# Performance work log

Hardware: AMD Instinct MI355X
Metric: run time of the kernel (lower is better)

Reference implementation:

```python
import jax, jax.numpy as jnp
import numpy as np

BN_EPS = 1e-5

def _bn(h, g, b):
    # BatchNorm1d training-mode math: biased batch stats over the node axis.
    m = h.mean(axis=0)
    v = h.var(axis=0)
    return (h - m) * jax.lax.rsqrt(v + BN_EPS) * g + b

def setup_inputs() -> dict:
    key = jax.random.key(0)
    ks = jax.random.split(key, 8)
    N, E, D_IN, H, L = 50000, 800000, 128, 256, 3
    return {
        "x": jax.random.normal(ks[0], (N, D_IN), dtype=jnp.float32),
        "edge_index": jax.random.randint(ks[1], (2, E), 0, N, dtype=jnp.int64),
        "eps": jnp.zeros((L,), dtype=jnp.float32),
        "W1_0": jax.random.normal(ks[2], (D_IN, H), dtype=jnp.float32),
        "W1_rest": jax.random.normal(ks[3], (L - 1, H, H), dtype=jnp.float32),
        "b1": jnp.zeros((L, H), dtype=jnp.float32),
        "g1": jnp.ones((L, H), dtype=jnp.float32),
        "bt1": jnp.zeros((L, H), dtype=jnp.float32),
        "W2": jax.random.normal(ks[4], (L, H, H), dtype=jnp.float32),
        "b2": jnp.zeros((L, H), dtype=jnp.float32),
        "g2": jnp.ones((L, H), dtype=jnp.float32),
        "bt2": jnp.zeros((L, H), dtype=jnp.float32),
    }

def reference(x, edge_index, eps, W1_0, W1_rest, b1, g1, bt1, W2, b2, g2, bt2):
    N = x.shape[0]
    row, col = edge_index[0], edge_index[1]
    L = eps.shape[0]

    def gin_layer(h, eps_i, Wa, ba, ga, bta, Wb, bb, gb, btb):
        # sum_{u in N(v)} h_u : gather source feats, scatter-add to dest rows
        agg = jax.ops.segment_sum(h[col], row, num_segments=N)
        out = (1.0 + eps_i) * h + agg
        out = _bn(out @ Wa + ba, ga, bta)        # Linear -> BN
        out = jax.nn.relu(out)                    # ReLU
        out = _bn(out @ Wb + bb, gb, btb)        # Linear -> BN
        return out

    h = x
    for i in range(L):
        Wa = W1_0 if i == 0 else W1_rest[i - 1]
        h = gin_layer(h, eps[i], Wa, b1[i], g1[i], bt1[i], W2[i], b2[i], g2[i], bt2[i])
        if i < L - 1:
            h = jax.nn.relu(h)  # inter-layer ReLU; dropout is identity in eval mode
    return h
```

## Files before the change

### kernel.cpp

```cpp
#include <hip/hip_runtime.h>
#include <hip/hip_bf16.h>
#include <math.h>
#include <stdint.h>

typedef short short8 __attribute__((ext_vector_type(8)));
typedef float f32x4 __attribute__((ext_vector_type(4)));

__device__ __forceinline__ float bf2f(unsigned int u) {
    union { unsigned int i; float f; } x; x.i = u << 16; return x.f;
}
__device__ __forceinline__ unsigned short f2bf(float f) {
    union { float f; unsigned int i; } x; x.f = f;
    unsigned int r = x.i + 0x7fffu + ((x.i >> 16) & 1u);
    return (unsigned short)(r >> 16);
}

__global__ void zero_i(int* __restrict__ p, int n) {
    int i = blockIdx.x * blockDim.x + threadIdx.x;
    if (i < n) p[i] = 0;
}
__global__ void hist_k(const int* __restrict__ row, int* __restrict__ deg, int E) {
    int e = blockIdx.x * blockDim.x + threadIdx.x;
    if (e < E) atomicAdd(&deg[row[e]], 1);
}
__global__ void block_sums(const int* __restrict__ deg, int* __restrict__ bs, int N) {
    __shared__ int tmp[256];
    int t = threadIdx.x;
    int i = blockIdx.x * 256 + t;
    tmp[t] = (i < N) ? deg[i] : 0;
    __syncthreads();
    for (int off = 128; off > 0; off >>= 1) {
        if (t < off) tmp[t] += tmp[t + off];
        __syncthreads();
    }
    if (t == 0) bs[blockIdx.x] = tmp[0];
}
__global__ void scan_bs(const int* __restrict__ bs, int* __restrict__ bo, int B) {
    __shared__ int tmp[256];
    int t = threadIdx.x;
    int v = (t < B) ? bs[t] : 0;
    tmp[t] = v;
    __syncthreads();
    for (int off = 1; off < 256; off <<= 1) {
        int x = (t >= off) ? tmp[t - off] : 0;
        __syncthreads();
        tmp[t] += x;
        __syncthreads();
    }
    bo[t] = tmp[t] - v;
}
__global__ void finalize_rowptr(const int* __restrict__ deg, const int* __restrict__ bo,
                                int* __restrict__ rowptr, int* __restrict__ cursor,
                                int N, int E) {
    __shared__ int tmp[256];
    int t = threadIdx.x;
    int i = blockIdx.x * 256 + t;
    int v = (i < N) ? deg[i] : 0;
    tmp[t] = v;
    __syncthreads();
    for (int off = 1; off < 256; off <<= 1) {
        int x = (t >= off) ? tmp[t - off] : 0;
        __syncthreads();
        tmp[t] += x;
        __syncthreads();
    }
    int excl = tmp[t] - v + bo[blockIdx.x];
    if (i < N) { rowptr[i] = excl; cursor[i] = excl; }
    if (i == N) rowptr[N] = E;
}
__global__ void fill_csr(const int* __restrict__ row, const int* __restrict__ col,
                         int* __restrict__ cursor, int* __restrict__ idx, int E) {
    int e = blockIdx.x * blockDim.x + threadIdx.x;
    if (e < E) {
        int p = atomicAdd(&cursor[row[e]], 1);
        idx[p] = col[e];
    }
}

__global__ void zero3(uint4* a, int na, uint4* b, int nb, uint4* c, int nc) {
    int i = blockIdx.x * blockDim.x + threadIdx.x;
    uint4 z = make_uint4(0, 0, 0, 0);
    if (i < na) a[i] = z;
    if (i < nb) b[i] = z;
    if (i < nc) c[i] = z;
}

__global__ void conv_x(const float* __restrict__ x, unsigned short* __restrict__ xb, int total4) {
    int i = blockIdx.x * blockDim.x + threadIdx.x;
    if (i >= total4) return;
    float4 v = *(const float4*)(x + (size_t)i * 4);
    unsigned int lo = (unsigned int)f2bf(v.x) | ((unsigned int)f2bf(v.y) << 16);
    unsigned int hi = (unsigned int)f2bf(v.z) | ((unsigned int)f2bf(v.w) << 16);
    *(uint2*)(xb + (size_t)i * 4) = make_uint2(lo, hi);
}

__global__ void prep_weights(const float* __restrict__ W1_0, const float* __restrict__ W1rest,
                             const float* __restrict__ W2, unsigned short* __restrict__ wt) {
    int id = blockIdx.x * blockDim.x + threadIdx.x;
    if (id < 32768) {
        int k = id >> 8, c = id & 255;
        wt[c * 128 + k] = f2bf(W1_0[id]);
    } else if (id < 163840) {
        int t = id - 32768;
        int m = t >> 16, r = t & 65535;
        int k = r >> 8, c = r & 255;
        wt[32768 + m * 65536 + c * 256 + k] = f2bf(W1rest[t]);
    } else if (id < 360448) {
        int t = id - 163840;
        int m = t >> 16, r = t & 65535;
        int k = r >> 8, c = r & 255;
        wt[163840 + m * 65536 + c * 256 + k] = f2bf(W2[t]);
    }
}

__global__ void bnpar(const float* __restrict__ stats, const float* __restrict__ g,
                      const float* __restrict__ bt, float* __restrict__ par, float invN) {
    int c = threadIdx.x;
    float m = stats[c] * invN;
    float v = stats[256 + c] * invN - m * m;
    float s = g[c] * rsqrtf(v + 1e-5f);
    par[c] = s;
    par[256 + c] = bt[c] - m * s;
}

template<int H, bool FUSE_BN>
__global__ __launch_bounds__(256) void aggregate_f(
    const unsigned short* __restrict__ h,
    const int* __restrict__ rowptr, const int* __restrict__ idx,
    const float* __restrict__ eps_p, int layer,
    const float* __restrict__ par,
    unsigned short* __restrict__ out, int N) {
    constexpr int NW = H / 128;
    int lane = threadIdx.x & 63;
    int v = blockIdx.x * 4 + (threadIdx.x >> 6);
    if (v >= N) return;

    float sc[2 * NW], sh[2 * NW];
    if constexpr (FUSE_BN) {
#pragma unroll
        for (int j = 0; j < 2 * NW; ++j) {
            int c = lane * 2 * NW + j;
            sc[j] = par[c];
            sh[j] = par[256 + c];
        }
    }
    const float s = 1.f + eps_p[layer];
    const unsigned int* hu = (const unsigned int*)h;

    float acc[2 * NW];
    {
        const unsigned int* hv = hu + (size_t)v * (H / 2) + lane * NW;
#pragma unroll
        for (int j = 0; j < NW; ++j) {
            unsigned int r = hv[j];
            float f0 = bf2f(r & 0xffffu), f1 = bf2f(r >> 16);
            if constexpr (FUSE_BN) {
                f0 = fmaxf(f0 * sc[2 * j] + sh[2 * j], 0.f);
                f1 = fmaxf(f1 * sc[2 * j + 1] + sh[2 * j + 1], 0.f);
            }
            acc[2 * j] = s * f0;
            acc[2 * j + 1] = s * f1;
        }
    }
    int e = rowptr[v], end = rowptr[v + 1];
    for (; e + 7 < end; e += 8) {
        unsigned int r[8][NW];
#pragma unroll
        for (int k = 0; k < 8; ++k) {
            const unsigned int* q = hu + (size_t)idx[e + k] * (H / 2) + lane * NW;
#pragma unroll
            for (int j = 0; j < NW; ++j) r[k][j] = q[j];
        }
#pragma unroll
        for (int j = 0; j < NW; ++j) {
            float t0 = 0.f, t1 = 0.f;
#pragma unroll
            for (int k = 0; k < 8; ++k) {
                float f0 = bf2f(r[k][j] & 0xffffu), f1 = bf2f(r[k][j] >> 16);
                if constexpr (FUSE_BN) {
                    f0 = fmaxf(f0 * sc[2 * j] + sh[2 * j], 0.f);
                    f1 = fmaxf(f1 * sc[2 * j + 1] + sh[2 * j + 1], 0.f);
                }
                t0 += f0; t1 += f1;
            }
            acc[2 * j] += t0;
            acc[2 * j + 1] += t1;
        }
    }
    for (; e + 3 < end; e += 4) {
        unsigned int r[4][NW];
#pragma unroll
        for (int k = 0; k < 4; ++k) {
            const unsigned int* q = hu + (size_t)idx[e + k] * (H / 2) + lane * NW;
#pragma unroll
            for (int j = 0; j < NW; ++j) r[k][j] = q[j];
        }
#pragma unroll
        for (int j = 0; j < NW; ++j) {
            float t0 = 0.f, t1 = 0.f;
#pragma unroll
            for (int k = 0; k < 4; ++k) {
                float f0 = bf2f(r[k][j] & 0xffffu), f1 = bf2f(r[k][j] >> 16);
                if constexpr (FUSE_BN) {
                    f0 = fmaxf(f0 * sc[2 * j] + sh[2 * j], 0.f);
                    f1 = fmaxf(f1 * sc[2 * j + 1] + sh[2 * j + 1], 0.f);
                }
                t0 += f0; t1 += f1;
            }
            acc[2 * j] += t0;
            acc[2 * j + 1] += t1;
        }
    }
    for (; e < end; ++e) {
        const unsigned int* q = hu + (size_t)idx[e] * (H / 2) + lane * NW;
#pragma unroll
        for (int j = 0; j < NW; ++j) {
            unsigned int r = q[j];
            float f0 = bf2f(r & 0xffffu), f1 = bf2f(r >> 16);
            if constexpr (FUSE_BN) {
                f0 = fmaxf(f0 * sc[2 * j] + sh[2 * j], 0.f);
                f1 = fmaxf(f1 * sc[2 * j + 1] + sh[2 * j + 1], 0.f);
            }
            acc[2 * j] += f0;
            acc[2 * j + 1] += f1;
        }
    }
    unsigned int* op = (unsigned int*)out + (size_t)v * (H / 2) + lane * NW;
#pragma unroll
    for (int j = 0; j < NW; ++j)
        op[j] = (unsigned int)f2bf(acc[2 * j]) | ((unsigned int)f2bf(acc[2 * j + 1]) << 16);
}

template<int K, bool TRANS_A>
__global__ __launch_bounds__(256) void gemm_mfma(const unsigned short* __restrict__ A,
                                                 const unsigned short* __restrict__ Wt,
                                                 const float* __restrict__ bias,
                                                 const float* __restrict__ par,
                                                 unsigned short* __restrict__ Y,
                                                 float* __restrict__ stats,
                                                 int Nrows) {
    __shared__ unsigned short sA[2][128 * 32];
    __shared__ unsigned short sB[2][128 * 32];
    __shared__ float reds[128], redq[128];
    const int tid = threadIdx.x;
    const int lane = tid & 63;
    const int wid = tid >> 6;
    const int wm = wid >> 1, wn = wid & 1;
    const int r0 = blockIdx.x * 128;
    const int c0 = blockIdx.y * 128;
    const int chunk0 = wid * 2;
    const int akk = (lane & 3) * 8;
    const int arow_l = lane >> 2;

    f32x4 acc[4][4] = {};

    auto stageB = [&](int buf, int k0) {
#pragma unroll
        for (int q = 0; q < 2; ++q) {
            int chunk = chunk0 + q;
            int byteoff = chunk * 1024 + lane * 16;
            int row = byteoff >> 6;
            int kk = (byteoff & 63) >> 1;
            const unsigned short* gB = Wt + (size_t)(c0 + row) * K + k0 + kk;
            __builtin_amdgcn_global_load_lds(
                (const __attribute__((address_space(1))) void*)(uintptr_t)gB,
                (__attribute__((address_space(3))) void*)(uintptr_t)(&sB[buf][chunk * 512]),
                16, 0, 0);
        }
    };
    auto stageA_direct = [&](int buf, int k0) {
#pragma unroll
        for (int q = 0; q < 2; ++q) {
            int chunk = chunk0 + q;
            int byteoff = chunk * 1024 + lane * 16;
            int row = byteoff >> 6;
            int kk = (byteoff & 63) >> 1;
            const unsigned short* gA = A + (size_t)(r0 + row) * K + k0 + kk;
            __builtin_amdgcn_global_load_lds(
                (const __attribute__((address_space(1))) void*)(uintptr_t)gA,
                (__attribute__((address_space(3))) void*)(uintptr_t)(&sA[buf][chunk * 512]),
                16, 0, 0);
        }
    };
    uint4 areg[2];
    auto loadA = [&](int k0) {
#pragma unroll
        for (int q = 0; q < 2; ++q) {
            int row = (chunk0 + q) * 16 + arow_l;
            areg[q] = *(const uint4*)(A + (size_t)(r0 + row) * K + k0 + akk);
        }
    };
    auto writeA = [&](int buf, int k0) {
        float4 sca = *(const float4*)&par[k0 + akk];
        float4 scb = *(const float4*)&par[k0 + akk + 4];
        float4 sha = *(const float4*)&par[256 + k0 + akk];
        float4 shb = *(const float4*)&par[256 + k0 + akk + 4];
#pragma unroll
        for (int q = 0; q < 2; ++q) {
            uint4 u = areg[q];
            float f0 = fmaxf(bf2f(u.x & 0xffffu) * sca.x + sha.x, 0.f);
            float f1 = fmaxf(bf2f(u.x >> 16)     * sca.y + sha.y, 0.f);
            float f2 = fmaxf(bf2f(u.y & 0xffffu) * sca.z + sha.z, 0.f);
            float f3 = fmaxf(bf2f(u.y >> 16)     * sca.w + sha.w, 0.f);
            float f4 = fmaxf(bf2f(u.z & 0xffffu) * scb.x + shb.x, 0.f);
            float f5 = fmaxf(bf2f(u.z >> 16)     * scb.y + shb.y, 0.f);
            float f6 = fmaxf(bf2f(u.w & 0xffffu) * scb.z + shb.z, 0.f);
            float f7 = fmaxf(bf2f(u.w >> 16)     * scb.w + shb.w, 0.f);
            uint4 w;
            w.x = (unsigned int)f2bf(f0) | ((unsigned int)f2bf(f1) << 16);
            w.y = (unsigned int)f2bf(f2) | ((unsigned int)f2bf(f3) << 16);
            w.z = (unsigned int)f2bf(f4) | ((unsigned int)f2bf(f5) << 16);
            w.w = (unsigned int)f2bf(f6) | ((unsigned int)f2bf(f7) << 16);
            *(uint4*)&sA[buf][(chunk0 + q) * 512 + lane * 8] = w;
        }
    };

    const int nt = K / 32;
    if constexpr (TRANS_A) { loadA(0); } else { stageA_direct(0, 0); }
    stageB(0, 0);
    const int krow = lane >> 4;
    const int rl = lane & 15;

    for (int t = 0; t < nt; ++t) {
        if constexpr (TRANS_A) writeA(t & 1, t * 32);
        __syncthreads();
        if (t + 1 < nt) {
            stageB((t + 1) & 1, (t + 1) * 32);
            if constexpr (TRANS_A) loadA((t + 1) * 32);
            else stageA_direct((t + 1) & 1, (t + 1) * 32);
        }
        const unsigned short* sAb = sA[t & 1];
        const unsigned short* sBb = sB[t & 1];
        short8 a[4], b[4];
#pragma unroll
        for (int i = 0; i < 4; ++i) {
            a[i] = *(const short8*)(sAb + (wm * 64 + i * 16 + rl) * 32 + krow * 8);
            b[i] = *(const short8*)(sBb + (wn * 64 + i * 16 + rl) * 32 + krow * 8);
        }
#pragma unroll
        for (int i = 0; i < 4; ++i)
#pragma unroll
            for (int n = 0; n < 4; ++n)
                asm volatile("v_mfma_f32_16x16x32_bf16 %0, %1, %2, %0"
                             : "+v"(acc[i][n])
                             : "v"(a[i]), "v"(b[n]));
    }
    asm volatile("s_nop 7\n\ts_nop 7" ::);

    const int rg = lane >> 4;
    float ssum[4], qsum[4];
#pragma unroll
    for (int n = 0; n < 4; ++n) {
        int col = c0 + wn * 64 + n * 16 + rl;
        float bv = bias[col];
        float s = 0.f, q2 = 0.f;
#pragma unroll
        for (int i = 0; i < 4; ++i) {
#pragma unroll
            for (int r = 0; r < 4; ++r) {
                int grow = r0 + wm * 64 + i * 16 + rg * 4 + r;
                if (grow < Nrows) {
                    float v = acc[i][n][r] + bv;
                    Y[(size_t)grow * 256 + col] = f2bf(v);
                    s += v;
                    q2 += v * v;
                }
            }
        }
        s  += __shfl_xor(s, 16, 64);  s  += __shfl_xor(s, 32, 64);
        q2 += __shfl_xor(q2, 16, 64); q2 += __shfl_xor(q2, 32, 64);
        ssum[n] = s; qsum[n] = q2;
    }
    if (wm == 0 && rg == 0) {
#pragma unroll
        for (int n = 0; n < 4; ++n) {
            int lc = wn * 64 + n * 16 + rl;
            reds[lc] = ssum[n];
            redq[lc] = qsum[n];
        }
    }
    __syncthreads();
    if (wm == 1 && rg == 0) {
#pragma unroll
        for (int n = 0; n < 4; ++n) {
            int lc = wn * 64 + n * 16 + rl;
            int c = c0 + lc;
            atomicAdd(&stats[c], ssum[n] + reds[lc]);
            atomicAdd(&stats[256 + c], qsum[n] + redq[lc]);
        }
    }
}

__global__ void bn_fuse(const unsigned short* __restrict__ Y, const float* __restrict__ stats,
                        const float* __restrict__ g, const float* __restrict__ bt,
                        float invN, float* __restrict__ outf, int total8) {
    int i = blockIdx.x * blockDim.x + threadIdx.x;
    if (i >= total8) return;
    int col0 = (i & 31) << 3;
    uint4 y = ((const uint4*)Y)[i];
    unsigned int yy[4] = {y.x, y.y, y.z, y.w};
    float o[8];
#pragma unroll
    for (int j = 0; j < 4; ++j) {
        o[2 * j]     = bf2f(yy[j] & 0xffffu);
        o[2 * j + 1] = bf2f(yy[j] >> 16);
    }
#pragma unroll
    for (int j = 0; j < 8; ++j) {
        int c = col0 + j;
        float mean = stats[c] * invN;
        float var = stats[256 + c] * invN - mean * mean;
        float sc = g[c] * rsqrtf(var + 1e-5f);
        float sh = bt[c] - mean * sc;
        o[j] = o[j] * sc + sh;
    }
    float4* of = (float4*)outf;
    of[2 * i]     = make_float4(o[0], o[1], o[2], o[3]);
    of[2 * i + 1] = make_float4(o[4], o[5], o[6], o[7]);
}

extern "C" void kernel_launch(void* const* d_in, const int* in_sizes, int n_in,
                              void* d_out, int out_size, void* d_ws, size_t ws_size,
                              hipStream_t stream) {
    const float* x      = (const float*)d_in[0];
    const int*   ei     = (const int*)d_in[1];
    const float* eps    = (const float*)d_in[2];
    const float* W1_0   = (const float*)d_in[3];
    const float* W1rest = (const float*)d_in[4];
    const float* b1     = (const float*)d_in[5];
    const float* g1     = (const float*)d_in[6];
    const float* bt1    = (const float*)d_in[7];
    const float* W2     = (const float*)d_in[8];
    const float* b2     = (const float*)d_in[9];
    const float* g2     = (const float*)d_in[10];
    const float* bt2    = (const float*)d_in[11];

    const int N = in_sizes[0] / 128;
    const int E = in_sizes[1] / 2;
    const int* row = ei;
    const int* col = ei + E;
    const int Npad = ((N + 127) / 128) * 128;
    const int nbRow = Npad / 128;

    char* w = (char*)d_ws;
    auto alloc = [&](size_t bytes) {
        char* p = w;
        w += (bytes + 255) & ~(size_t)255;
        return p;
    };
    unsigned short* xb = (unsigned short*)alloc((size_t)Npad * 128 * 2);
    unsigned short* p0 = (unsigned short*)alloc((size_t)Npad * 256 * 2);
    unsigned short* p1 = (unsigned short*)alloc((size_t)Npad * 256 * 2);
    unsigned short* Yb = (unsigned short*)alloc((size_t)Npad * 256 * 2);
    unsigned short* wt = (unsigned short*)alloc((size_t)360448 * 2);
    float* stats  = (float*)alloc(3072 * 4);
    float* params = (float*)alloc(3072 * 4);
    int* deg    = (int*)alloc((size_t)N * 4);
    int* cursor = (int*)alloc((size_t)N * 4);
    int* rowptr = (int*)alloc((size_t)(N + 1) * 4);
    int* bs     = (int*)alloc(256 * 4);
    int* bo     = (int*)alloc(256 * 4);
    int* idxb   = (int*)alloc((size_t)E * 4);

    const float invN = 1.f / (float)N;
    const int B = (N + 255) / 256;

    zero_i<<<(N + 255) / 256, 256, 0, stream>>>(deg, N);
    hist_k<<<(E + 255) / 256, 256, 0, stream>>>(row, deg, E);
    block_sums<<<B, 256, 0, stream>>>(deg, bs, N);
    scan_bs<<<1, 256, 0, stream>>>(bs, bo, B);
    finalize_rowptr<<<B, 256, 0, stream>>>(deg, bo, rowptr, cursor, N, E);
    fill_csr<<<(E + 255) / 256, 256, 0, stream>>>(row, col, cursor, idxb, E);

    int tail16 = (Npad - N) * 256 * 2 / 16;
    {
        uint4* t0 = (uint4*)(p0 + (size_t)N * 256);
        uint4* t1 = (uint4*)(p1 + (size_t)N * 256);
        int mx = tail16 > 768 ? tail16 : 768;
        zero3<<<(mx + 255) / 256, 256, 0, stream>>>(t0, tail16, t1, tail16, (uint4*)stats, 768);
    }

    conv_x<<<(N * 32 + 255) / 256, 256, 0, stream>>>(x, xb, N * 32);
    prep_weights<<<(360448 + 255) / 256, 256, 0, stream>>>(W1_0, W1rest, W2, wt);

    const int aggGrid = (N + 3) / 4;
    const int bnGrid = (N * 32 + 255) / 256;
    dim3 gg(nbRow, 2);

    for (int layer = 0; layer < 3; ++layer) {
        float* st1 = stats + layer * 1024;
        float* st2 = st1 + 512;
        float* pr1 = params + layer * 1024;
        float* pr2 = pr1 + 512;

        if (layer == 0)
            aggregate_f<128, false><<<aggGrid, 256, 0, stream>>>(
                xb, rowptr, idxb, eps, 0, nullptr, p1, N);
        else
            aggregate_f<256, true><<<aggGrid, 256, 0, stream>>>(
                p0, rowptr, idxb, eps, layer, params + (layer - 1) * 1024 + 512, p1, N);

        if (layer == 0)
            gemm_mfma<128, false><<<gg, 256, 0, stream>>>(p1, wt, b1, nullptr, Yb, st1, N);
        else
            gemm_mfma<256, false><<<gg, 256, 0, stream>>>(
                p1, wt + 32768 + (size_t)(layer - 1) * 65536, b1 + layer * 256, nullptr, Yb, st1, N);

        bnpar<<<1, 256, 0, stream>>>(st1, g1 + layer * 256, bt1 + layer * 256, pr1, invN);

        gemm_mfma<256, true><<<gg, 256, 0, stream>>>(
            Yb, wt + 163840 + (size_t)layer * 65536, b2 + layer * 256, pr1, p0, st2, N);

        if (layer < 2)
            bnpar<<<1, 256, 0, stream>>>(st2, g2 + layer * 256, bt2 + layer * 256, pr2, invN);
        else
            bn_fuse<<<bnGrid, 256, 0, stream>>>(p0, st2, g2 + layer * 256, bt2 + layer * 256,
                                                invN, (float*)d_out, N * 32);
    }
}
```

Baseline: 515.6 us.

## Reorder GIN layers to transform then aggregate, fusing BN into GEMM loads

```diff
diff --git a/kernel.cpp b/kernel.cpp
--- a/kernel.cpp
+++ b/kernel.cpp
@@ -15,10 +15,6 @@
     return (unsigned short)(r >> 16);
 }
 
-__global__ void zero_i(int* __restrict__ p, int n) {
-    int i = blockIdx.x * blockDim.x + threadIdx.x;
-    if (i < n) p[i] = 0;
-}
 __global__ void hist_k(const int* __restrict__ row, int* __restrict__ deg, int E) {
     int e = blockIdx.x * blockDim.x + threadIdx.x;
     if (e < E) atomicAdd(&deg[row[e]], 1);
@@ -77,26 +73,28 @@
     }
 }
 
-__global__ void zero3(uint4* a, int na, uint4* b, int nb, uint4* c, int nc) {
+__global__ void zero_all(int* __restrict__ deg, int n_deg,
+                         uint4* __restrict__ a, uint4* __restrict__ b, uint4* __restrict__ c,
+                         int n_t, uint4* __restrict__ st, int n_st) {
     int i = blockIdx.x * blockDim.x + threadIdx.x;
     uint4 z = make_uint4(0, 0, 0, 0);
-    if (i < na) a[i] = z;
-    if (i < nb) b[i] = z;
-    if (i < nc) c[i] = z;
-}
-
-__global__ void conv_x(const float* __restrict__ x, unsigned short* __restrict__ xb, int total4) {
+    if (i < n_deg) deg[i] = 0;
+    if (i < n_t) { a[i] = z; b[i] = z; c[i] = z; }
+    if (i < n_st) st[i] = z;
+}
+
+__global__ void prep_all(const float* __restrict__ x, unsigned short* __restrict__ xb, int nconv,
+                         const float* __restrict__ W1_0, const float* __restrict__ W1rest,
+                         const float* __restrict__ W2, unsigned short* __restrict__ wt) {
     int i = blockIdx.x * blockDim.x + threadIdx.x;
-    if (i >= total4) return;
-    float4 v = *(const float4*)(x + (size_t)i * 4);
-    unsigned int lo = (unsigned int)f2bf(v.x) | ((unsigned int)f2bf(v.y) << 16);
-    unsigned int hi = (unsigned int)f2bf(v.z) | ((unsigned int)f2bf(v.w) << 16);
-    *(uint2*)(xb + (size_t)i * 4) = make_uint2(lo, hi);
-}
-
-__global__ void prep_weights(const float* __restrict__ W1_0, const float* __restrict__ W1rest,
-                             const float* __restrict__ W2, unsigned short* __restrict__ wt) {
-    int id = blockIdx.x * blockDim.x + threadIdx.x;
+    if (i < nconv) {
+        float4 v = *(const float4*)(x + (size_t)i * 4);
+        unsigned int lo = (unsigned int)f2bf(v.x) | ((unsigned int)f2bf(v.y) << 16);
+        unsigned int hi = (unsigned int)f2bf(v.z) | ((unsigned int)f2bf(v.w) << 16);
+        *(uint2*)(xb + (size_t)i * 4) = make_uint2(lo, hi);
+        return;
+    }
+    int id = i - nconv;
     if (id < 32768) {
         int k = id >> 8, c = id & 255;
         wt[c * 128 + k] = f2bf(W1_0[id]);
@@ -113,135 +111,118 @@
     }
 }
 
-__global__ void bnpar(const float* __restrict__ stats, const float* __restrict__ g,
-                      const float* __restrict__ bt, float* __restrict__ par, float invN) {
-    int c = threadIdx.x;
-    float m = stats[c] * invN;
-    float v = stats[256 + c] * invN - m * m;
-    float s = g[c] * rsqrtf(v + 1e-5f);
-    par[c] = s;
-    par[256 + c] = bt[c] - m * s;
-}
-
-template<int H, bool FUSE_BN>
-__global__ __launch_bounds__(256) void aggregate_f(
+template<int H, bool STATS>
+__global__ __launch_bounds__(256) void aggregate_s(
     const unsigned short* __restrict__ h,
     const int* __restrict__ rowptr, const int* __restrict__ idx,
     const float* __restrict__ eps_p, int layer,
-    const float* __restrict__ par,
-    unsigned short* __restrict__ out, int N) {
+    const float* __restrict__ bias,
+    unsigned short* __restrict__ out,
+    float* __restrict__ stats, int N) {
     constexpr int NW = H / 128;
-    int lane = threadIdx.x & 63;
-    int v = blockIdx.x * 4 + (threadIdx.x >> 6);
-    if (v >= N) return;
-
-    float sc[2 * NW], sh[2 * NW];
-    if constexpr (FUSE_BN) {
+    constexpr int NPW = 8;
+    __shared__ float lsum[512];
+    const int tid = threadIdx.x;
+    const int lane = tid & 63;
+    const int wave = tid >> 6;
+    if constexpr (STATS) {
+        if (tid < 256) { lsum[tid] = 0.f; lsum[256 + tid] = 0.f; }
+        __syncthreads();
+    }
+    const float s = 1.f + eps_p[layer];
+    const unsigned int* hu = (const unsigned int*)h;
+
+    float bv[2 * NW];
+    if constexpr (STATS) {
+#pragma unroll
+        for (int j = 0; j < 2 * NW; ++j) bv[j] = bias[lane * 2 * NW + j];
+    }
+    float ssum[2 * NW] = {}, qsum[2 * NW] = {};
+
+    const int v0 = (blockIdx.x * 4 + wave) * NPW;
+    for (int vi = 0; vi < NPW; ++vi) {
+        int v = v0 + vi;
+        if (v < N) {
+            float acc[2 * NW];
+            {
+                const unsigned int* hv = hu + (size_t)v * (H / 2) + lane * NW;
+#pragma unroll
+                for (int j = 0; j < NW; ++j) {
+                    unsigned int r = hv[j];
+                    acc[2 * j] = s * bf2f(r & 0xffffu);
+                    acc[2 * j + 1] = s * bf2f(r >> 16);
+                }
+            }
+            int e = rowptr[v], end = rowptr[v + 1];
+            for (; e + 3 < end; e += 4) {
+                int u0 = idx[e], u1 = idx[e + 1], u2 = idx[e + 2], u3 = idx[e + 3];
+                const unsigned int* q0 = hu + (size_t)u0 * (H / 2) + lane * NW;
+                const unsigned int* q1 = hu + (size_t)u1 * (H / 2) + lane * NW;
+                const unsigned int* q2 = hu + (size_t)u2 * (H / 2) + lane * NW;
+                const unsigned int* q3 = hu + (size_t)u3 * (H / 2) + lane * NW;
+                unsigned int r0[NW], r1[NW], r2[NW], r3[NW];
+#pragma unroll
+                for (int j = 0; j < NW; ++j) { r0[j] = q0[j]; r1[j] = q1[j]; r2[j] = q2[j]; r3[j] = q3[j]; }
+#pragma unroll
+                for (int j = 0; j < NW; ++j) {
+                    acc[2 * j]     += (bf2f(r0[j] & 0xffffu) + bf2f(r1[j] & 0xffffu)) +
+                                      (bf2f(r2[j] & 0xffffu) + bf2f(r3[j] & 0xffffu));
+                    acc[2 * j + 1] += (bf2f(r0[j] >> 16) + bf2f(r1[j] >> 16)) +
+                                      (bf2f(r2[j] >> 16) + bf2f(r3[j] >> 16));
+                }
+            }
+            for (; e < end; ++e) {
+                const unsigned int* q = hu + (size_t)idx[e] * (H / 2) + lane * NW;
+#pragma unroll
+                for (int j = 0; j < NW; ++j) {
+                    unsigned int r = q[j];
+                    acc[2 * j] += bf2f(r & 0xffffu);
+                    acc[2 * j + 1] += bf2f(r >> 16);
+                }
+            }
+            unsigned int* op = (unsigned int*)out + (size_t)v * (H / 2) + lane * NW;
+#pragma unroll
+            for (int j = 0; j < NW; ++j) {
+                float f0 = acc[2 * j], f1 = acc[2 * j + 1];
+                if constexpr (STATS) {
+                    f0 += bv[2 * j]; f1 += bv[2 * j + 1];
+                    ssum[2 * j] += f0; qsum[2 * j] += f0 * f0;
+                    ssum[2 * j + 1] += f1; qsum[2 * j + 1] += f1 * f1;
+                }
+                op[j] = (unsigned int)f2bf(f0) | ((unsigned int)f2bf(f1) << 16);
+            }
+        }
+    }
+    if constexpr (STATS) {
 #pragma unroll
         for (int j = 0; j < 2 * NW; ++j) {
             int c = lane * 2 * NW + j;
-            sc[j] = par[c];
-            sh[j] = par[256 + c];
-        }
-    }
-    const float s = 1.f + eps_p[layer];
-    const unsigned int* hu = (const unsigned int*)h;
-
-    float acc[2 * NW];
-    {
-        const unsigned int* hv = hu + (size_t)v * (H / 2) + lane * NW;
-#pragma unroll
-        for (int j = 0; j < NW; ++j) {
-            unsigned int r = hv[j];
-            float f0 = bf2f(r & 0xffffu), f1 = bf2f(r >> 16);
-            if constexpr (FUSE_BN) {
-                f0 = fmaxf(f0 * sc[2 * j] + sh[2 * j], 0.f);
-                f1 = fmaxf(f1 * sc[2 * j + 1] + sh[2 * j + 1], 0.f);
-            }
-            acc[2 * j] = s * f0;
-            acc[2 * j + 1] = s * f1;
-        }
-    }
-    int e = rowptr[v], end = rowptr[v + 1];
-    for (; e + 7 < end; e += 8) {
-        unsigned int r[8][NW];
-#pragma unroll
-        for (int k = 0; k < 8; ++k) {
-            const unsigned int* q = hu + (size_t)idx[e + k] * (H / 2) + lane * NW;
-#pragma unroll
-            for (int j = 0; j < NW; ++j) r[k][j] = q[j];
-        }
-#pragma unroll
-        for (int j = 0; j < NW; ++j) {
-            float t0 = 0.f, t1 = 0.f;
-#pragma unroll
-            for (int k = 0; k < 8; ++k) {
-                float f0 = bf2f(r[k][j] & 0xffffu), f1 = bf2f(r[k][j] >> 16);
-                if constexpr (FUSE_BN) {
-                    f0 = fmaxf(f0 * sc[2 * j] + sh[2 * j], 0.f);
-                    f1 = fmaxf(f1 * sc[2 * j + 1] + sh[2 * j + 1], 0.f);
-                }
-                t0 += f0; t1 += f1;
-            }
-            acc[2 * j] += t0;
-            acc[2 * j + 1] += t1;
-        }
-    }
-    for (; e + 3 < end; e += 4) {
-        unsigned int r[4][NW];
-#pragma unroll
-        for (int k = 0; k < 4; ++k) {
-            const unsigned int* q = hu + (size_t)idx[e + k] * (H / 2) + lane * NW;
-#pragma unroll
-            for (int j = 0; j < NW; ++j) r[k][j] = q[j];
-        }
-#pragma unroll
-        for (int j = 0; j < NW; ++j) {
-            float t0 = 0.f, t1 = 0.f;
-#pragma unroll
-            for (int k = 0; k < 4; ++k) {
-                float f0 = bf2f(r[k][j] & 0xffffu), f1 = bf2f(r[k][j] >> 16);
-                if constexpr (FUSE_BN) {
-                    f0 = fmaxf(f0 * sc[2 * j] + sh[2 * j], 0.f);
-                    f1 = fmaxf(f1 * sc[2 * j + 1] + sh[2 * j + 1], 0.f);
-                }
-                t0 += f0; t1 += f1;
-            }
-            acc[2 * j] += t0;
-            acc[2 * j + 1] += t1;
-        }
-    }
-    for (; e < end; ++e) {
-        const unsigned int* q = hu + (size_t)idx[e] * (H / 2) + lane * NW;
-#pragma unroll
-        for (int j = 0; j < NW; ++j) {
-            unsigned int r = q[j];
-            float f0 = bf2f(r & 0xffffu), f1 = bf2f(r >> 16);
-            if constexpr (FUSE_BN) {
-                f0 = fmaxf(f0 * sc[2 * j] + sh[2 * j], 0.f);
-                f1 = fmaxf(f1 * sc[2 * j + 1] + sh[2 * j + 1], 0.f);
-            }
-            acc[2 * j] += f0;
-            acc[2 * j + 1] += f1;
-        }
-    }
-    unsigned int* op = (unsigned int*)out + (size_t)v * (H / 2) + lane * NW;
-#pragma unroll
-    for (int j = 0; j < NW; ++j)
-        op[j] = (unsigned int)f2bf(acc[2 * j]) | ((unsigned int)f2bf(acc[2 * j + 1]) << 16);
-}
-
-template<int K, bool TRANS_A>
+            atomicAdd(&lsum[c], ssum[j]);
+            atomicAdd(&lsum[256 + c], qsum[j]);
+        }
+        __syncthreads();
+        if (tid < 256) {
+            atomicAdd(&stats[tid], lsum[tid]);
+            atomicAdd(&stats[256 + tid], lsum[256 + tid]);
+        }
+    }
+}
+
+template<int K, bool TRANS_A, bool STATS>
 __global__ __launch_bounds__(256) void gemm_mfma(const unsigned short* __restrict__ A,
                                                  const unsigned short* __restrict__ Wt,
                                                  const float* __restrict__ bias,
-                                                 const float* __restrict__ par,
+                                                 const float* __restrict__ stats_in,
+                                                 const float* __restrict__ gp,
+                                                 const float* __restrict__ btp,
+                                                 float invN,
                                                  unsigned short* __restrict__ Y,
-                                                 float* __restrict__ stats,
+                                                 float* __restrict__ stats_out,
                                                  int Nrows) {
     __shared__ unsigned short sA[2][128 * 32];
     __shared__ unsigned short sB[2][128 * 32];
     __shared__ float reds[128], redq[128];
+    __shared__ float spc[256], sps[256];
     const int tid = threadIdx.x;
     const int lane = tid & 63;
     const int wid = tid >> 6;
@@ -251,6 +232,15 @@
     const int chunk0 = wid * 2;
     const int akk = (lane & 3) * 8;
     const int arow_l = lane >> 2;
+
+    if constexpr (TRANS_A) {
+        float m = stats_in[tid] * invN;
+        float var = stats_in[256 + tid] * invN - m * m;
+        float sv = gp[tid] * rsqrtf(var + 1e-5f);
+        spc[tid] = sv;
+        sps[tid] = btp[tid] - m * sv;
+        __syncthreads();
+    }
 
     f32x4 acc[4][4] = {};
 
@@ -291,10 +281,10 @@
         }
     };
     auto writeA = [&](int buf, int k0) {
-        float4 sca = *(const float4*)&par[k0 + akk];
-        float4 scb = *(const float4*)&par[k0 + akk + 4];
-        float4 sha = *(const float4*)&par[256 + k0 + akk];
-        float4 shb = *(const float4*)&par[256 + k0 + akk + 4];
+        float4 sca = *(const float4*)&spc[k0 + akk];
+        float4 scb = *(const float4*)&spc[k0 + akk + 4];
+        float4 sha = *(const float4*)&sps[k0 + akk];
+        float4 shb = *(const float4*)&sps[k0 + akk + 4];
 #pragma unroll
         for (int q = 0; q < 2; ++q) {
             uint4 u = areg[q];
@@ -348,45 +338,61 @@
     asm volatile("s_nop 7\n\ts_nop 7" ::);
 
     const int rg = lane >> 4;
-    float ssum[4], qsum[4];
-#pragma unroll
-    for (int n = 0; n < 4; ++n) {
-        int col = c0 + wn * 64 + n * 16 + rl;
-        float bv = bias[col];
-        float s = 0.f, q2 = 0.f;
-#pragma unroll
-        for (int i = 0; i < 4; ++i) {
-#pragma unroll
-            for (int r = 0; r < 4; ++r) {
-                int grow = r0 + wm * 64 + i * 16 + rg * 4 + r;
-                if (grow < Nrows) {
-                    float v = acc[i][n][r] + bv;
-                    Y[(size_t)grow * 256 + col] = f2bf(v);
-                    s += v;
-                    q2 += v * v;
+    if constexpr (STATS) {
+        float ssum[4], qsum[4];
+#pragma unroll
+        for (int n = 0; n < 4; ++n) {
+            int col = c0 + wn * 64 + n * 16 + rl;
+            float bvv = bias[col];
+            float s = 0.f, q2 = 0.f;
+#pragma unroll
+            for (int i = 0; i < 4; ++i) {
+#pragma unroll
+                for (int r = 0; r < 4; ++r) {
+                    int grow = r0 + wm * 64 + i * 16 + rg * 4 + r;
+                    if (grow < Nrows) {
+                        float v = acc[i][n][r] + bvv;
+                        Y[(size_t)grow * 256 + col] = f2bf(v);
+                        s += v;
+                        q2 += v * v;
+                    }
                 }
             }
-        }
-        s  += __shfl_xor(s, 16, 64);  s  += __shfl_xor(s, 32, 64);
-        q2 += __shfl_xor(q2, 16, 64); q2 += __shfl_xor(q2, 32, 64);
-        ssum[n] = s; qsum[n] = q2;
-    }
-    if (wm == 0 && rg == 0) {
+            s  += __shfl_xor(s, 16, 64);  s  += __shfl_xor(s, 32, 64);
+            q2 += __shfl_xor(q2, 16, 64); q2 += __shfl_xor(q2, 32, 64);
+            ssum[n] = s; qsum[n] = q2;
+        }
+        if (wm == 0 && rg == 0) {
+#pragma unroll
+            for (int n = 0; n < 4; ++n) {
+                int lc = wn * 64 + n * 16 + rl;
+                reds[lc] = ssum[n];
+                redq[lc] = qsum[n];
+            }
+        }
+        __syncthreads();
+        if (wm == 1 && rg == 0) {
+#pragma unroll
+            for (int n = 0; n < 4; ++n) {
+                int lc = wn * 64 + n * 16 + rl;
+                int c = c0 + lc;
+                atomicAdd(&stats_out[c], ssum[n] + reds[lc]);
+                atomicAdd(&stats_out[256 + c], qsum[n] + redq[lc]);
+            }
+        }
+    } else {
 #pragma unroll
         for (int n = 0; n < 4; ++n) {
-            int lc = wn * 64 + n * 16 + rl;
-            reds[lc] = ssum[n];
-            redq[lc] = qsum[n];
-        }
-    }
-    __syncthreads();
-    if (wm == 1 && rg == 0) {
-#pragma unroll
-        for (int n = 0; n < 4; ++n) {
-            int lc = wn * 64 + n * 16 + rl;
-            int c = c0 + lc;
-            atomicAdd(&stats[c], ssum[n] + reds[lc]);
-            atomicAdd(&stats[256 + c], qsum[n] + redq[lc]);
+            int col = c0 + wn * 64 + n * 16 + rl;
+#pragma unroll
+            for (int i = 0; i < 4; ++i) {
+#pragma unroll
+                for (int r = 0; r < 4; ++r) {
+                    int grow = r0 + wm * 64 + i * 16 + rg * 4 + r;
+                    if (grow < Nrows)
+                        Y[(size_t)grow * 256 + col] = f2bf(acc[i][n][r]);
+                }
+            }
         }
     }
 }
@@ -454,7 +460,6 @@
     unsigned short* Yb = (unsigned short*)alloc((size_t)Npad * 256 * 2);
     unsigned short* wt = (unsigned short*)alloc((size_t)360448 * 2);
     float* stats  = (float*)alloc(3072 * 4);
-    float* params = (float*)alloc(3072 * 4);
     int* deg    = (int*)alloc((size_t)N * 4);
     int* cursor = (int*)alloc((size_t)N * 4);
     int* rowptr = (int*)alloc((size_t)(N + 1) * 4);
@@ -465,56 +470,57 @@
     const float invN = 1.f / (float)N;
     const int B = (N + 255) / 256;
 
-    zero_i<<<(N + 255) / 256, 256, 0, stream>>>(deg, N);
+    int tail16 = (Npad - N) * 256 * 2 / 16;
+    {
+        uint4* t0 = (uint4*)(p0 + (size_t)N * 256);
+        uint4* t1 = (uint4*)(p1 + (size_t)N * 256);
+        uint4* t2 = (uint4*)(Yb + (size_t)N * 256);
+        int mx = N;
+        if (tail16 > mx) mx = tail16;
+        if (768 > mx) mx = 768;
+        zero_all<<<(mx + 255) / 256, 256, 0, stream>>>(deg, N, t0, t1, t2, tail16,
+                                                       (uint4*)stats, 768);
+    }
+
     hist_k<<<(E + 255) / 256, 256, 0, stream>>>(row, deg, E);
     block_sums<<<B, 256, 0, stream>>>(deg, bs, N);
     scan_bs<<<1, 256, 0, stream>>>(bs, bo, B);
     finalize_rowptr<<<B, 256, 0, stream>>>(deg, bo, rowptr, cursor, N, E);
     fill_csr<<<(E + 255) / 256, 256, 0, stream>>>(row, col, cursor, idxb, E);
 
-    int tail16 = (Npad - N) * 256 * 2 / 16;
-    {
-        uint4* t0 = (uint4*)(p0 + (size_t)N * 256);
-        uint4* t1 = (uint4*)(p1 + (size_t)N * 256);
-        int mx = tail16 > 768 ? tail16 : 768;
-        zero3<<<(mx + 255) / 256, 256, 0, stream>>>(t0, tail16, t1, tail16, (uint4*)stats, 768);
-    }
-
-    conv_x<<<(N * 32 + 255) / 256, 256, 0, stream>>>(x, xb, N * 32);
-    prep_weights<<<(360448 + 255) / 256, 256, 0, stream>>>(W1_0, W1rest, W2, wt);
-
-    const int aggGrid = (N + 3) / 4;
+    const int nconv = N * 32;
+    prep_all<<<(nconv + 360448 + 255) / 256, 256, 0, stream>>>(x, xb, nconv,
+                                                               W1_0, W1rest, W2, wt);
+
+    const int aggGrid = (N + 31) / 32;
     const int bnGrid = (N * 32 + 255) / 256;
     dim3 gg(nbRow, 2);
 
-    for (int layer = 0; layer < 3; ++layer) {
+    aggregate_s<128, false><<<aggGrid, 256, 0, stream>>>(
+        xb, rowptr, idxb, eps, 0, nullptr, p1, nullptr, N);
+    gemm_mfma<128, false, true><<<gg, 256, 0, stream>>>(
+        p1, wt, b1, nullptr, nullptr, nullptr, invN, Yb, stats, N);
+    gemm_mfma<256, true, true><<<gg, 256, 0, stream>>>(
+        Yb, wt + 163840, b2, stats, g1, bt1, invN, p0, stats + 512, N);
+
+    for (int layer = 1; layer < 3; ++layer) {
         float* st1 = stats + layer * 1024;
         float* st2 = st1 + 512;
-        float* pr1 = params + layer * 1024;
-        float* pr2 = pr1 + 512;
-
-        if (layer == 0)
-            aggregate_f<128, false><<<aggGrid, 256, 0, stream>>>(
-                xb, rowptr, idxb, eps, 0, nullptr, p1, N);
-        else
-            aggregate_f<256, true><<<aggGrid, 256, 0, stream>>>(
-                p0, rowptr, idxb, eps, layer, params + (layer - 1) * 1024 + 512, p1, N);
-
-        if (layer == 0)
-            gemm_mfma<128, false><<<gg, 256, 0, stream>>>(p1, wt, b1, nullptr, Yb, st1, N);
-        else
-            gemm_mfma<256, false><<<gg, 256, 0, stream>>>(
-                p1, wt + 32768 + (size_t)(layer - 1) * 65536, b1 + layer * 256, nullptr, Yb, st1, N);
-
-        bnpar<<<1, 256, 0, stream>>>(st1, g1 + layer * 256, bt1 + layer * 256, pr1, invN);
-
-        gemm_mfma<256, true><<<gg, 256, 0, stream>>>(
-            Yb, wt + 163840 + (size_t)layer * 65536, b2 + layer * 256, pr1, p0, st2, N);
-
-        if (layer < 2)
-            bnpar<<<1, 256, 0, stream>>>(st2, g2 + layer * 256, bt2 + layer * 256, pr2, invN);
-        else
-            bn_fuse<<<bnGrid, 256, 0, stream>>>(p0, st2, g2 + layer * 256, bt2 + layer * 256,
-                                                invN, (float*)d_out, N * 32);
-    }
-}
+        float* st2p = stats + (layer - 1) * 1024 + 512;
+
+        gemm_mfma<256, true, false><<<gg, 256, 0, stream>>>(
+            p0, wt + 32768 + (size_t)(layer - 1) * 65536, nullptr,
+            st2p, g2 + (layer - 1) * 256, bt2 + (layer - 1) * 256, invN, Yb, nullptr, N);
+
+        aggregate_s<256, true><<<aggGrid, 256, 0, stream>>>(
+            Yb, rowptr, idxb, eps, layer, b1 + layer * 256, p1, st1, N);
+
+        gemm_mfma<256, true, true><<<gg, 256, 0, stream>>>(
+            p1, wt + 163840 + (size_t)layer * 65536, b2 + layer * 256,
+            st1, g1 + layer * 256, bt1 + layer * 256, invN, p0, st2, N);
+    }
+
+    bn_fuse<<<bnGrid, 256, 0, stream>>>(p0, stats + 2 * 1024 + 512,
+                                        g2 + 2 * 256, bt2 + 2 * 256,
+                                        invN, (float*)d_out, N * 32);
+}
```

Result: slower. 548.4 us (+6.4%).
